# Kernel tuning notes

Hardware: AMD Instinct MI355X
Metric: run time of the kernel (lower is better)

Reference implementation:

```python
import jax, jax.numpy as jnp
import numpy as np

SMOOTH = 1.0

def setup_inputs() -> dict:
    key = jax.random.key(0)
    k1, k2 = jax.random.split(key)
    shape = (2, 4, 64, 256, 256)  # [B, organs, D, H, W]
    predict = jax.random.normal(k1, shape, dtype=jnp.float32)
    target = jax.random.uniform(k2, shape, dtype=jnp.float32)
    return {"predict": predict, "target": target}

def reference(predict, target):
    # sigmoid over whole prediction tensor (done once in DiceLoss.forward)
    p = jax.nn.sigmoid(predict)
    B, O, D = p.shape[0], p.shape[1], p.shape[2]
    # BinaryDiceLoss views each [D, H, W] organ slice as (D, H*W):
    pf = p.reshape(B, O, D, -1)
    tf = target.reshape(B, O, D, -1)
    num = jnp.sum(pf * tf, axis=-1)                      # [B, O, D]
    den = jnp.sum(pf, axis=-1) + jnp.sum(tf, axis=-1) + SMOOTH
    dice_loss = 1.0 - 2.0 * num / den                    # [B, O, D]
    # slices with first element == -1 are ignored
    valid = (tf[..., 0] != -1).astype(dice_loss.dtype)   # [B, O, D]
    per_slice_avg = jnp.sum(dice_loss * valid, axis=-1) / jnp.sum(valid, axis=-1)  # [B, O]
    # outer loop averages over all B*4 (b, organ) pairs
    return jnp.mean(per_slice_avg)
```

## Files before the change

### kernel.cpp

```cpp
#include <hip/hip_runtime.h>


constexpr int HW       = 256 * 256;
constexpr int NSLICE   = 2 * 4 * 64;
constexpr int NPAIR    = 2 * 4;
constexpr int THREADS  = 1024;
constexpr int ITERS    = (HW / 4) / THREADS;
constexpr int BATCH    = 8;

__global__ __launch_bounds__(THREADS) void dice_stage1(
    const float* __restrict__ predict,
    const float* __restrict__ target,
    float* __restrict__ ws)
{
    const int slice = blockIdx.x;
    const int tid   = threadIdx.x;
    const size_t base = (size_t)slice * HW;
    const float4* __restrict__ p4 = (const float4*)(predict + base);
    const float4* __restrict__ t4 = (const float4*)(target + base);

    float s_pt0 = 0.f, s_pt1 = 0.f, s_p0 = 0.f, s_p1 = 0.f, s_t0 = 0.f, s_t1 = 0.f;

    for (int k0 = 0; k0 < ITERS; k0 += BATCH) {
        float4 pv[BATCH], tv[BATCH];
#pragma unroll
        for (int j = 0; j < BATCH; ++j)
            pv[j] = p4[(size_t)(k0 + j) * THREADS + tid];
#pragma unroll
        for (int j = 0; j < BATCH; ++j)
            tv[j] = t4[(size_t)(k0 + j) * THREADS + tid];
#pragma unroll
        for (int j = 0; j < BATCH; ++j) {
            float e0 = 1.f / (1.f + __expf(-pv[j].x));
            float e1 = 1.f / (1.f + __expf(-pv[j].y));
            float e2 = 1.f / (1.f + __expf(-pv[j].z));
            float e3 = 1.f / (1.f + __expf(-pv[j].w));
            s_pt0 += e0 * tv[j].x + e1 * tv[j].y;
            s_pt1 += e2 * tv[j].z + e3 * tv[j].w;
            s_p0  += e0 + e1;
            s_p1  += e2 + e3;
            s_t0  += tv[j].x + tv[j].y;
            s_t1  += tv[j].z + tv[j].w;
        }
    }

    float s_pt = s_pt0 + s_pt1;
    float s_p  = s_p0 + s_p1;
    float s_t  = s_t0 + s_t1;

#pragma unroll
    for (int off = 32; off > 0; off >>= 1) {
        s_pt += __shfl_down(s_pt, off, 64);
        s_p  += __shfl_down(s_p,  off, 64);
        s_t  += __shfl_down(s_t,  off, 64);
    }

    __shared__ float l_pt[THREADS / 64];
    __shared__ float l_p [THREADS / 64];
    __shared__ float l_t [THREADS / 64];
    const int wave = tid >> 6;
    const int lane = tid & 63;
    if (lane == 0) { l_pt[wave] = s_pt; l_p[wave] = s_p; l_t[wave] = s_t; }
    __syncthreads();

    if (tid == 0) {
        float num = 0.f, sp = 0.f, st = 0.f;
#pragma unroll
        for (int w = 0; w < THREADS / 64; ++w) {
            num += l_pt[w]; sp += l_p[w]; st += l_t[w];
        }
        float den  = sp + st + 1.0f;
        float dice = 1.0f - 2.0f * num / den;
        float valid = (target[base] != -1.0f) ? 1.0f : 0.0f;
        ws[slice]          = dice * valid;
        ws[NSLICE + slice] = valid;
    }
}

__global__ __launch_bounds__(NSLICE) void dice_stage2(
    const float* __restrict__ ws, float* __restrict__ out)
{
    const int tid = threadIdx.x;
    float dv = ws[tid];
    float v  = ws[NSLICE + tid];
#pragma unroll
    for (int off = 32; off > 0; off >>= 1) {
        dv += __shfl_down(dv, off, 64);
        v  += __shfl_down(v,  off, 64);
    }
    __shared__ float pair_avg[NPAIR];
    const int wave = tid >> 6;
    const int lane = tid & 63;
    if (lane == 0) pair_avg[wave] = dv / v;
    __syncthreads();
    if (tid == 0) {
        float s = 0.f;
#pragma unroll
        for (int w = 0; w < NPAIR; ++w) s += pair_avg[w];
        out[0] = s * (1.0f / NPAIR);
    }
}

extern "C" void kernel_launch(void* const* d_in, const int* in_sizes, int n_in,
                              void* d_out, int out_size, void* d_ws, size_t ws_size,
                              hipStream_t stream) {
    const float* predict = (const float*)d_in[0];
    const float* target  = (const float*)d_in[1];
    float* ws  = (float*)d_ws;
    float* out = (float*)d_out;

    dice_stage1<<<NSLICE, THREADS, 0, stream>>>(predict, target, ws);
    dice_stage2<<<1, NSLICE, 0, stream>>>(ws, out);
}
```

Measured before the change: 278.1 us.

## Split each slice across four smaller blocks and finish dice in stage two

Stage one now launches four 256-thread blocks per slice instead of one 1024-thread block. Each block writes raw partial sums, and stage two combines the chunks, computes dice, and checks validity. A sched_barrier is added after the loads so they stay grouped ahead of the compute. The aim is finer-grained scheduling and better wave balance across CUs for a bandwidth-bound reduction, at the cost of three times the workspace traffic and a longer stage two.

```diff
diff --git a/kernel.cpp b/kernel.cpp
--- a/kernel.cpp
+++ b/kernel.cpp
@@ -4,31 +4,37 @@
 constexpr int HW       = 256 * 256;
 constexpr int NSLICE   = 2 * 4 * 64;
 constexpr int NPAIR    = 2 * 4;
-constexpr int THREADS  = 1024;
-constexpr int ITERS    = (HW / 4) / THREADS;
+constexpr int CHUNKS   = 4;
+constexpr int NBLOCK   = NSLICE * CHUNKS;
+constexpr int THREADS  = 256;
+constexpr int CHUNK_F4 = HW / 4 / CHUNKS;
+constexpr int ITERS    = CHUNK_F4 / THREADS;
 constexpr int BATCH    = 8;
+constexpr int OUTER    = ITERS / BATCH;
 
-__global__ __launch_bounds__(THREADS) void dice_stage1(
+
+__global__ __launch_bounds__(THREADS, 2) void dice_stage1(
     const float* __restrict__ predict,
     const float* __restrict__ target,
     float* __restrict__ ws)
 {
-    const int slice = blockIdx.x;
-    const int tid   = threadIdx.x;
-    const size_t base = (size_t)slice * HW;
-    const float4* __restrict__ p4 = (const float4*)(predict + base);
-    const float4* __restrict__ t4 = (const float4*)(target + base);
+    const int blk = blockIdx.x;
+    const int tid = threadIdx.x;
+    const size_t base4 = (size_t)blk * CHUNK_F4;
+    const float4* __restrict__ p4 = (const float4*)predict + base4;
+    const float4* __restrict__ t4 = (const float4*)target  + base4;
 
     float s_pt0 = 0.f, s_pt1 = 0.f, s_p0 = 0.f, s_p1 = 0.f, s_t0 = 0.f, s_t1 = 0.f;
 
-    for (int k0 = 0; k0 < ITERS; k0 += BATCH) {
+    for (int it = 0; it < OUTER; ++it) {
         float4 pv[BATCH], tv[BATCH];
 #pragma unroll
         for (int j = 0; j < BATCH; ++j)
-            pv[j] = p4[(size_t)(k0 + j) * THREADS + tid];
+            pv[j] = p4[(it * BATCH + j) * THREADS + tid];
 #pragma unroll
         for (int j = 0; j < BATCH; ++j)
-            tv[j] = t4[(size_t)(k0 + j) * THREADS + tid];
+            tv[j] = t4[(it * BATCH + j) * THREADS + tid];
+        __builtin_amdgcn_sched_barrier(0);
 #pragma unroll
         for (int j = 0; j < BATCH; ++j) {
             float e0 = 1.f / (1.f + __expf(-pv[j].x));
@@ -64,25 +70,37 @@
     __syncthreads();
 
     if (tid == 0) {
-        float num = 0.f, sp = 0.f, st = 0.f;
+        float pt = 0.f, sp = 0.f, st = 0.f;
 #pragma unroll
         for (int w = 0; w < THREADS / 64; ++w) {
-            num += l_pt[w]; sp += l_p[w]; st += l_t[w];
+            pt += l_pt[w]; sp += l_p[w]; st += l_t[w];
         }
-        float den  = sp + st + 1.0f;
-        float dice = 1.0f - 2.0f * num / den;
-        float valid = (target[base] != -1.0f) ? 1.0f : 0.0f;
-        ws[slice]          = dice * valid;
-        ws[NSLICE + slice] = valid;
+        ws[blk]              = pt;
+        ws[NBLOCK + blk]     = sp;
+        ws[2 * NBLOCK + blk] = st;
     }
 }
 
 __global__ __launch_bounds__(NSLICE) void dice_stage2(
-    const float* __restrict__ ws, float* __restrict__ out)
+    const float* __restrict__ ws,
+    const float* __restrict__ target,
+    float* __restrict__ out)
 {
     const int tid = threadIdx.x;
-    float dv = ws[tid];
-    float v  = ws[NSLICE + tid];
+    float pt = 0.f, sp = 0.f, st = 0.f;
+#pragma unroll
+    for (int c = 0; c < CHUNKS; ++c) {
+        const int i = tid * CHUNKS + c;
+        pt += ws[i];
+        sp += ws[NBLOCK + i];
+        st += ws[2 * NBLOCK + i];
+    }
+    const float valid = (target[(size_t)tid * HW] != -1.0f) ? 1.0f : 0.0f;
+    const float den   = sp + st + 1.0f;
+    const float dice  = 1.0f - 2.0f * pt / den;
+
+    float dv = dice * valid;
+    float v  = valid;
 #pragma unroll
     for (int off = 32; off > 0; off >>= 1) {
         dv += __shfl_down(dv, off, 64);
@@ -109,6 +127,6 @@
     float* ws  = (float*)d_ws;
     float* out = (float*)d_out;
 
-    dice_stage1<<<NSLICE, THREADS, 0, stream>>>(predict, target, ws);
-    dice_stage2<<<1, NSLICE, 0, stream>>>(ws, out);
+    dice_stage1<<<NBLOCK, THREADS, 0, stream>>>(predict, target, ws);
+    dice_stage2<<<1, NSLICE, 0, stream>>>(ws, target, out);
 }
```

Measured after the change: 278.3 us. No clear change (+0.1%).
